# Optimization experiments

Hardware: AMD Instinct MI355X
Metric: run time of the kernel (lower is better)

The kernel has to match this reference:

```python
import jax, jax.numpy as jnp
import numpy as np

B, N, DIM = 8, 8192, 256
K, CDIM = 4096, 1024
COMMIT = 0.25


def setup_inputs() -> dict:
    key = jax.random.key(0)
    ks = jax.random.split(key, 4)
    x = jax.random.normal(ks[0], (B, N, DIM), dtype=jnp.float32)
    ln_g = jnp.ones((DIM,), jnp.float32)
    ln_b = jnp.zeros((DIM,), jnp.float32)
    w_pre = jax.random.normal(ks[1], (DIM, CDIM), jnp.float32) / np.sqrt(DIM)
    b_pre = jnp.zeros((CDIM,), jnp.float32)
    embed = jax.random.normal(ks[2], (K, CDIM), jnp.float32)
    w_post = jax.random.normal(ks[3], (CDIM, DIM), jnp.float32) / np.sqrt(CDIM)
    b_post = jnp.zeros((DIM,), jnp.float32)
    return {"x": x, "ln_g": ln_g, "ln_b": ln_b, "w_pre": w_pre, "b_pre": b_pre,
            "embed": embed, "w_post": w_post, "b_post": b_post}


def reference(x, ln_g, ln_b, w_pre, b_pre, embed, w_post, b_post):
    # LayerNorm over last dim (eps=1e-5, torch default)
    mu = jnp.mean(x, axis=-1, keepdims=True)
    var = jnp.mean((x - mu) ** 2, axis=-1, keepdims=True)
    xn = (x - mu) * jax.lax.rsqrt(var + 1e-5) * ln_g + ln_b
    # GELU (exact, erf-based as in torch default) then Linear dim->codebook_dim
    z_e = jax.nn.gelu(xn, approximate=False) @ w_pre + b_pre  # (B,N,CDIM)
    flat = z_e.reshape(-1, CDIM)                              # (B*N, CDIM)
    # squared euclidean distances to codebook, argmin, gather
    z_sq = jnp.sum(flat * flat, axis=1, keepdims=True)        # (BN,1)
    e_sq = jnp.sum(embed * embed, axis=1)                     # (K,)
    dist = z_sq - 2.0 * (flat @ embed.T) + e_sq[None, :]      # (BN,K)
    indices = jnp.argmin(dist, axis=1)                        # (BN,)
    z_q = embed[indices]                                      # (BN,CDIM)
    # commitment loss (z_q detached)
    commit = COMMIT * jnp.mean((flat - jax.lax.stop_gradient(z_q)) ** 2)
    # straight-through estimator
    z_q_st = flat + jax.lax.stop_gradient(z_q - flat)
    z_q_st = z_q_st.reshape(B, N, CDIM)
    quantized = z_q_st @ w_post + b_post                      # (B,N,DIM)
    return quantized, indices.reshape(B, N), commit
```

## Files before the change

kernel.cpp:

```cpp
#include <hip/hip_runtime.h>

#define BN_ROWS 65536
#define DIMX 256
#define CDIM 1024
#define KCODES 4096
#define NSP 16
#define NSLOT 11
#define NENT 12
#define CMARG 24.0f
#define RMARG 24.0f
#define QS 24.0f
#define INV_S2 (1.0f / (QS * QS))
#define FLT_BIG 3.402823466e+38f

static const size_t OFF_ESQ   = 0;
static const size_t OFF_IDXF  = 16384;
static const size_t OFF_CROW  = 278528;
static const size_t OFF_EPOST = 540672;
static const size_t OFF_EI8   = 4734976;
static const size_t OFF_NFLAG = 8929280;
static const size_t OFF_FLAG  = 8929344;
static const size_t OFF_CAND  = 9191488;

typedef __attribute__((ext_vector_type(4))) int i32x4;

#define GLOAD_LDS16(gsrc, ldst)                                                \
  __builtin_amdgcn_global_load_lds(                                            \
      (const __attribute__((address_space(1))) void*)(gsrc),                   \
      (__attribute__((address_space(3))) void*)(ldst), 16, 0, 0)

template <int VMC>
__device__ __forceinline__ void wait_vm() {
  if constexpr (VMC == 8)
    asm volatile("s_waitcnt vmcnt(8)" ::: "memory");
  else if constexpr (VMC == 4)
    asm volatile("s_waitcnt vmcnt(4)" ::: "memory");
  else
    asm volatile("s_waitcnt vmcnt(0)" ::: "memory");
}

__device__ inline char q8(float f) {
  return (char)__float2int_rn(fminf(fmaxf(f * QS, -127.f), 127.f));
}
__device__ inline unsigned fkey(float s) {
  unsigned b = __float_as_uint(s);
  return b ^ ((unsigned)((int)b >> 31) | 0x80000000u);
}
__device__ inline float keyinv(unsigned k) {
  unsigned b = (k & 0x80000000u) ? (k ^ 0x80000000u) : ~k;
  return __uint_as_float(b);
}

__global__ __launch_bounds__(256) void k_esq(const float* __restrict__ embed,
                                             float* __restrict__ e_sq) {
  const int t = threadIdx.x, wv = t >> 6, lane = t & 63;
  const int row = blockIdx.x * 4 + wv;
  const float* e = embed + (size_t)row * CDIM;
  float s = 0.f;
  for (int k = lane * 4; k < CDIM; k += 256) {
    float4 v = *(const float4*)(e + k);
    s = fmaf(v.x, v.x, s); s = fmaf(v.y, v.y, s);
    s = fmaf(v.z, v.z, s); s = fmaf(v.w, v.w, s);
  }
#pragma unroll
  for (int o = 32; o > 0; o >>= 1) s += __shfl_xor(s, o);
  if (lane == 0) e_sq[row] = s;
}

__global__ __launch_bounds__(256) void k_ei8(const float* __restrict__ embed,
                                             char* __restrict__ Ei8) {
  const int t = threadIdx.x;
  const size_t row = blockIdx.x;
  float4 v = *(const float4*)(embed + row * CDIM + t * 4);
  *(char4*)(Ei8 + row * CDIM + t * 4) =
      make_char4(q8(v.x), q8(v.y), q8(v.z), q8(v.w));
}

__global__ __launch_bounds__(256) void k_ln_gelu_gemm(
    const float* __restrict__ x, const float* __restrict__ ln_g,
    const float* __restrict__ ln_b, const float* __restrict__ w_pre,
    const float* __restrict__ b_pre, float* __restrict__ zf,
    char* __restrict__ zi8, int row0) {
  __shared__ float g[16][DIMX];
  const int t = threadIdx.x;
  const int lrow0 = blockIdx.x * 16;
  const int grow0 = row0 + lrow0;
  const int wv = t >> 6, lane = t & 63;
#pragma unroll
  for (int j = 0; j < 4; ++j) {
    const int r = wv * 4 + j;
    const float* xr = x + (size_t)(grow0 + r) * DIMX;
    float4 v = *(const float4*)(xr + lane * 4);
    float s = v.x + v.y + v.z + v.w;
    float ss = v.x * v.x + v.y * v.y + v.z * v.z + v.w * v.w;
#pragma unroll
    for (int o = 32; o > 0; o >>= 1) { s += __shfl_xor(s, o); ss += __shfl_xor(ss, o); }
    const float mu = s * (1.0f / 256.0f);
    const float var = ss * (1.0f / 256.0f) - mu * mu;
    const float rstd = rsqrtf(var + 1e-5f);
    float vv[4] = {v.x, v.y, v.z, v.w};
#pragma unroll
    for (int q = 0; q < 4; ++q) {
      const int d = lane * 4 + q;
      float xn = (vv[q] - mu) * rstd * ln_g[d] + ln_b[d];
      g[r][d] = 0.5f * xn * (1.0f + erff(xn * 0.70710678118654752f));
    }
  }
  __syncthreads();
  float acc[16][4];
#pragma unroll
  for (int r = 0; r < 16; ++r)
#pragma unroll
    for (int c = 0; c < 4; ++c) acc[r][c] = 0.f;
#pragma unroll 4
  for (int d = 0; d < DIMX; ++d) {
    float4 w = *(const float4*)(w_pre + (size_t)d * CDIM + t * 4);
#pragma unroll
    for (int r = 0; r < 16; ++r) {
      const float gv = g[r][d];
      acc[r][0] = fmaf(gv, w.x, acc[r][0]);
      acc[r][1] = fmaf(gv, w.y, acc[r][1]);
      acc[r][2] = fmaf(gv, w.z, acc[r][2]);
      acc[r][3] = fmaf(gv, w.w, acc[r][3]);
    }
  }
  float4 bp = *(const float4*)(b_pre + t * 4);
#pragma unroll
  for (int r = 0; r < 16; ++r) {
    float4 o;
    o.x = acc[r][0] + bp.x; o.y = acc[r][1] + bp.y;
    o.z = acc[r][2] + bp.z; o.w = acc[r][3] + bp.w;
    *(float4*)(zf + (size_t)(lrow0 + r) * CDIM + t * 4) = o;
    *(char4*)(zi8 + (size_t)(lrow0 + r) * CDIM + t * 4) =
        make_char4(q8(o.x), q8(o.y), q8(o.z), q8(o.w));
  }
}

__global__ __launch_bounds__(512) void k_score(
    const char* __restrict__ Ei8, const char* __restrict__ Zi8,
    const float* __restrict__ e_sq, uint2* __restrict__ cand, int chunk) {
  __shared__ __align__(16) char lds[4][32768];
  const int t = threadIdx.x;
  const int cpx = gridDim.x >> 3;
  const int bx = (blockIdx.x & 7) * cpx + (blockIdx.x >> 3);
  const int zblk = bx / NSP, csp = bx % NSP;
  const int wid = t >> 6, l = t & 63;
  const int wr = wid >> 2, wc = wid & 3;
  const int lg = l >> 4, lo16 = l & 15;
  const int rowbase = zblk * 256;
  const int m0 = csp * 256;
  const int wr8 = wr * 8, wc4 = wc * 4, l16 = l * 16;

  const bool isA = (wid < 4);
  const int q = wid & 3;
  const char* sarr = isA ? Ei8 : Zi8;
  const int sbase = isA ? m0 : rowbase;
  const char* sp0 = sarr + (size_t)(sbase + q * 64 + lo16) * 1024 + lg * 16;
  const int dstbase = (isA ? 0 : 16384) + q * 4096;

  i32x4 acc[8][4];
#pragma unroll
  for (int mi = 0; mi < 8; ++mi)
#pragma unroll
    for (int ni = 0; ni < 4; ++ni) acc[mi][ni] = (i32x4){0, 0, 0, 0};

#pragma unroll
  for (int pk = 0; pk < 3; ++pk) {
    const char* sp = sp0 + pk * 64;
    char* D = &lds[pk][dstbase];
#pragma unroll
    for (int u = 0; u < 4; ++u) GLOAD_LDS16(sp + u * 16384, D + u * 1024);
  }

#define SCORE_KT(KT, VMC, ST)                                                  \
  {                                                                            \
    const char* Lc = lds[(KT) & 3];                                            \
    wait_vm<VMC>();                                                            \
    __builtin_amdgcn_s_barrier();                                              \
    __builtin_amdgcn_sched_barrier(0);                                         \
    i32x4 bh[4], a[8];                                                         \
    _Pragma("unroll") for (int ni = 0; ni < 4; ++ni) bh[ni] =                  \
        *(const i32x4*)(Lc + 16384 + (wc4 + ni) * 1024 + l16);                 \
    _Pragma("unroll") for (int u = 0; u < 8; ++u) a[u] =                       \
        *(const i32x4*)(Lc + (wr8 + u) * 1024 + l16);                          \
    if (ST) {                                                                  \
      char* Dst = &lds[((KT) + 3) & 3][dstbase];                               \
      const char* spk = sp0 + ((KT) + 3) * 64;                                 \
      _Pragma("unroll") for (int u = 0; u < 4; ++u)                            \
          GLOAD_LDS16(spk + u * 16384, Dst + u * 1024);                        \
    }                                                                          \
    asm volatile("s_waitcnt lgkmcnt(0)" ::: "memory");                         \
    __builtin_amdgcn_sched_barrier(0);                                         \
    __builtin_amdgcn_s_setprio(1);                                             \
    _Pragma("unroll") for (int u = 0; u < 8; ++u)                              \
        _Pragma("unroll") for (int ni = 0; ni < 4; ++ni) acc[u][ni] =          \
            __builtin_amdgcn_mfma_i32_16x16x64_i8(a[u], bh[ni],                \
                                                  acc[u][ni], 0, 0, 0);        \
    __builtin_amdgcn_s_setprio(0);                                             \
  }

  for (int kt = 0; kt < 14; ++kt) SCORE_KT(kt, 8, (kt < 13));
  SCORE_KT(14, 4, false);
  SCORE_KT(15, 0, false);
#undef SCORE_KT

  float s1[4];
  int i1[4];
#pragma unroll
  for (int i = 0; i < 4; ++i) { s1[i] = FLT_BIG; i1[i] = 0x7fffffff; }
#pragma unroll
  for (int mi = 0; mi < 8; ++mi) {
    const int c0 = m0 + wr * 128 + mi * 16 + lg * 4;
    float4 es = *(const float4*)(e_sq + c0);
    float esv[4] = {es.x, es.y, es.z, es.w};
#pragma unroll
    for (int ni = 0; ni < 4; ++ni) {
#pragma unroll
      for (int j = 0; j < 4; ++j) {
        const float s = fmaf(-2.0f * INV_S2, (float)acc[mi][ni][j], esv[j]);
        const int c = c0 + j;
        if (s < s1[ni] || (s == s1[ni] && c < i1[ni])) { s1[ni] = s; i1[ni] = c; }
      }
    }
  }

  unsigned long long* red = (unsigned long long*)&lds[0][0];
  float* sb = (float*)&lds[0][4096];
  unsigned* sbi = (unsigned*)&lds[0][5120];
  unsigned* cnt = (unsigned*)&lds[0][6144];
  uint2* slot = (uint2*)&lds[0][7168];

  __syncthreads();
#pragma unroll
  for (int ni = 0; ni < 4; ++ni) {
    unsigned long long k1v =
        (((unsigned long long)fkey(s1[ni])) << 32) | (unsigned)i1[ni];
    unsigned long long o1 = __shfl_xor(k1v, 16);
    k1v = o1 < k1v ? o1 : k1v;
    o1 = __shfl_xor(k1v, 32);
    k1v = o1 < k1v ? o1 : k1v;
    if (lg == 0) {
      const int r = wc * 64 + ni * 16 + lo16;
      red[r * 2 + wr] = k1v;
    }
  }
  __syncthreads();
  if (t < 256) {
    unsigned long long a1 = red[t * 2 + 0], b1 = red[t * 2 + 1];
    if (b1 < a1) a1 = b1;
    sb[t] = keyinv((unsigned)(a1 >> 32));
    sbi[t] = (unsigned)(a1 & 0xFFFFFFFFull);
    cnt[t] = 0;
  }
  __syncthreads();
#pragma unroll
  for (int mi = 0; mi < 8; ++mi) {
    const int c0 = m0 + wr * 128 + mi * 16 + lg * 4;
    float4 es = *(const float4*)(e_sq + c0);
    float esv[4] = {es.x, es.y, es.z, es.w};
#pragma unroll
    for (int ni = 0; ni < 4; ++ni) {
      const int r = wc * 64 + ni * 16 + lo16;
      const float thr = sb[r] + CMARG;
#pragma unroll
      for (int j = 0; j < 4; ++j) {
        const float s = fmaf(-2.0f * INV_S2, (float)acc[mi][ni][j], esv[j]);
        const unsigned c = (unsigned)(c0 + j);
        if (s < thr && c != sbi[r]) {
          unsigned pos = atomicAdd(&cnt[r], 1u);
          if (pos < NSLOT)
            slot[r * NSLOT + pos] = make_uint2(__float_as_uint(s), c);
        }
      }
    }
  }
  __syncthreads();
  if (t < 256) {
    uint2* g = cand + (size_t)(rowbase + t) * (NSP * NENT) + csp * NENT;
    const unsigned ov = (cnt[t] > NSLOT) ? 0x40000000u : 0u;
    g[0] = make_uint2(__float_as_uint(sb[t]), sbi[t] | ov);
    const unsigned n = cnt[t] > NSLOT ? NSLOT : cnt[t];
#pragma unroll
    for (int k = 0; k < NSLOT; ++k)
      g[1 + k] = (k < (int)n) ? slot[t * NSLOT + k]
                              : make_uint2(__float_as_uint(FLT_BIG), 0xFFFFFFFFu);
  }
}

__global__ __launch_bounds__(256) void k_refine(
    const uint2* __restrict__ cand, const float* __restrict__ zf,
    const float* __restrict__ embed, int* __restrict__ idxf,
    float* __restrict__ crow, float* __restrict__ out_idx,
    int* __restrict__ flag_rows, int* __restrict__ nflag, int chunk,
    int row0) {
  const int t = threadIdx.x, wid = t >> 6, l = t & 63;
  const int lrow = blockIdx.x * 4 + wid;
  if (lrow >= chunk) return;
  const int grow = row0 + lrow;
  const uint2* base = cand + (size_t)lrow * (NSP * NENT);
  const uint2 e0 = base[l];
  const uint2 e1 = base[64 + l];
  const uint2 e2 = base[128 + l];
  const bool is0 = (l % NENT) == 0;
  const bool is1 = ((l + 64) % NENT) == 0;
  const bool is2 = ((l + 128) % NENT) == 0;
  float gm = FLT_BIG;
  if (is0) gm = fminf(gm, __uint_as_float(e0.x));
  if (is1) gm = fminf(gm, __uint_as_float(e1.x));
  if (is2) gm = fminf(gm, __uint_as_float(e2.x));
#pragma unroll
  for (int o = 32; o > 0; o >>= 1) gm = fminf(gm, __shfl_xor(gm, o));
  const float thr = gm + RMARG;
  bool myovf = (is0 && (e0.y & 0x40000000u) && __uint_as_float(e0.x) < thr) ||
               (is1 && (e1.y & 0x40000000u) && __uint_as_float(e1.x) < thr) ||
               (is2 && (e2.y & 0x40000000u) && __uint_as_float(e2.x) < thr);
  const bool ovf = __any(myovf);

  float zv[16];
#pragma unroll
  for (int j = 0; j < 16; ++j) zv[j] = zf[(size_t)lrow * CDIM + l + 64 * j];

  double d1 = 1e300;
  int i1 = 0x7fffffff;
#define PROC(E)                                                                \
  {                                                                            \
    const float sc_ = __uint_as_float(E.x);                                    \
    const int id_ = (int)(E.y & 0xFFFFu);                                      \
    unsigned long long mask = __ballot(sc_ < thr && id_ < KCODES);             \
    while (mask) {                                                             \
      const int src = __ffsll((unsigned long long)mask) - 1;                   \
      mask &= mask - 1;                                                        \
      const int c = __shfl(id_, src);                                          \
      const float* e = embed + (size_t)c * CDIM;                               \
      double dd = 0.0;                                                         \
      _Pragma("unroll") for (int j = 0; j < 16; ++j) {                         \
        const double df = (double)zv[j] - (double)e[l + 64 * j];               \
        dd = fma(df, df, dd);                                                  \
      }                                                                        \
      _Pragma("unroll") for (int o = 32; o > 0; o >>= 1) dd +=                 \
          __shfl_xor(dd, o);                                                   \
      if (dd < d1 || (dd == d1 && c < i1)) { d1 = dd; i1 = c; }                \
    }                                                                          \
  }
  PROC(e0);
  PROC(e1);
  PROC(e2);
#undef PROC
  if (l == 0) {
    idxf[grow] = i1;
    out_idx[grow] = (float)i1;
    crow[grow] = (float)d1;
    if (ovf) {
      const int s = atomicAdd(nflag, 1);
      flag_rows[s] = lrow;
    }
  }
}

__global__ __launch_bounds__(256) void k_exact(
    const float* __restrict__ zf, const float* __restrict__ embed,
    const int* __restrict__ flag_rows, const int* __restrict__ nflag,
    int* __restrict__ idxf, float* __restrict__ crow,
    float* __restrict__ out_idx, int row0) {
  __shared__ double wd[4];
  __shared__ int wcidx[4];
  const int t = threadIdx.x;
  const int wid = t >> 6, l = t & 63;
  const int n = *nflag;

  for (int fi = blockIdx.x; fi < n; fi += gridDim.x) {
    const int lrow = flag_rows[fi];
    const int grow = row0 + lrow;
    float zr[16];
#pragma unroll
    for (int j = 0; j < 16; ++j) zr[j] = zf[(size_t)lrow * CDIM + l + 64 * j];
    double dmin = 1e300;
    int cmin = 0x7fffffff;
    for (int ci = 0; ci < 1024; ++ci) {
      const int c = wid * 1024 + ci;
      const float* e = embed + (size_t)c * CDIM;
      double dd = 0.0;
#pragma unroll
      for (int j = 0; j < 16; ++j) {
        const double df = (double)zr[j] - (double)e[l + 64 * j];
        dd = fma(df, df, dd);
      }
#pragma unroll
      for (int o = 32; o > 0; o >>= 1) dd += __shfl_xor(dd, o);
      if (dd < dmin) { dmin = dd; cmin = c; }
    }
    if (l == 0) { wd[wid] = dmin; wcidx[wid] = cmin; }
    __syncthreads();
    if (t == 0) {
      double dm = wd[0]; int cm = wcidx[0];
#pragma unroll
      for (int wv = 1; wv < 4; ++wv) {
        if (wd[wv] < dm || (wd[wv] == dm && wcidx[wv] < cm)) {
          dm = wd[wv]; cm = wcidx[wv];
        }
      }
      idxf[grow] = cm;
      out_idx[grow] = (float)cm;
      crow[grow] = (float)dm;
    }
    __syncthreads();
  }
}

__global__ __launch_bounds__(256) void k_epost(const float* __restrict__ E,
                                               const float* __restrict__ w_post,
                                               float* __restrict__ E_post) {
  __shared__ float es[16][128];
  const int t = threadIdx.x;
  const int r0 = blockIdx.x * 16;
  float acc[16];
#pragma unroll
  for (int r = 0; r < 16; ++r) acc[r] = 0.f;
  for (int k0 = 0; k0 < CDIM; k0 += 128) {
    __syncthreads();
#pragma unroll
    for (int p = 0; p < 2; ++p) {
      const int fl = (p * 256 + t) * 4;
      const int r = fl >> 7, kk = fl & 127;
      float4 v = *(const float4*)(E + (size_t)(r0 + r) * CDIM + k0 + kk);
      *(float4*)&es[r][kk] = v;
    }
    __syncthreads();
#pragma unroll 4
    for (int d = 0; d < 128; ++d) {
      const float w = w_post[(size_t)(k0 + d) * DIMX + t];
#pragma unroll
      for (int r = 0; r < 16; ++r) acc[r] = fmaf(es[r][d], w, acc[r]);
    }
  }
#pragma unroll
  for (int r = 0; r < 16; ++r)
    E_post[(size_t)(r0 + r) * DIMX + t] = acc[r];
}

__global__ __launch_bounds__(256) void k_gather(const float* __restrict__ E_post,
                                                const int* __restrict__ idx,
                                                const float* __restrict__ b_post,
                                                float* __restrict__ outq) {
  const int t = threadIdx.x;
  const int r0 = blockIdx.x * 16;
  const float bp = b_post[t];
#pragma unroll
  for (int i = 0; i < 16; ++i) {
    const int row = r0 + i;
    outq[(size_t)row * DIMX + t] = E_post[(size_t)idx[row] * DIMX + t] + bp;
  }
}

__global__ __launch_bounds__(256) void k_commit_final(
    const float* __restrict__ crow, float* __restrict__ out_commit) {
  const int t = threadIdx.x;
  double s = 0.0;
  for (int i = t; i < BN_ROWS; i += 256) s += (double)crow[i];
#pragma unroll
  for (int o = 32; o > 0; o >>= 1) s += __shfl_xor(s, o);
  __shared__ double wsum[4];
  if ((t & 63) == 0) wsum[t >> 6] = s;
  __syncthreads();
  if (t == 0)
    *out_commit = (float)(0.25 * (wsum[0] + wsum[1] + wsum[2] + wsum[3]) /
                          (65536.0 * 1024.0));
}

extern "C" void kernel_launch(void* const* d_in, const int* in_sizes, int n_in,
                              void* d_out, int out_size, void* d_ws,
                              size_t ws_size, hipStream_t stream) {
  const float* x = (const float*)d_in[0];
  const float* ln_g = (const float*)d_in[1];
  const float* ln_b = (const float*)d_in[2];
  const float* w_pre = (const float*)d_in[3];
  const float* b_pre = (const float*)d_in[4];
  const float* embed = (const float*)d_in[5];
  const float* w_post = (const float*)d_in[6];
  const float* b_post = (const float*)d_in[7];

  float* out = (float*)d_out;
  float* outq = out;
  float* out_idx = out + 16777216;
  float* out_commit = out + 16842752;

  char* ws = (char*)d_ws;
  float* e_sq = (float*)(ws + OFF_ESQ);
  int* idxf = (int*)(ws + OFF_IDXF);
  float* crow = (float*)(ws + OFF_CROW);
  float* E_post = (float*)(ws + OFF_EPOST);
  char* Ei8 = (char*)(ws + OFF_EI8);
  int* nflag = (int*)(ws + OFF_NFLAG);
  int* flag_rows = (int*)(ws + OFF_FLAG);

  int chunk = 4096;
  while (chunk < BN_ROWS &&
         OFF_CAND + (size_t)(chunk * 2) * 6656ull <= ws_size)
    chunk *= 2;
  uint2* cand = (uint2*)(ws + OFF_CAND);
  char* zi8 = ws + OFF_CAND + (size_t)chunk * 1536;
  float* zf = (float*)(ws + OFF_CAND + (size_t)chunk * 1536 +
                       (size_t)chunk * 1024);

  k_esq<<<KCODES / 4, 256, 0, stream>>>(embed, e_sq);
  k_ei8<<<KCODES, 256, 0, stream>>>(embed, Ei8);
  k_epost<<<KCODES / 16, 256, 0, stream>>>(embed, w_post, E_post);

  for (int row0 = 0; row0 < BN_ROWS; row0 += chunk) {
    hipMemsetAsync(nflag, 0, sizeof(int), stream);
    k_ln_gelu_gemm<<<chunk / 16, 256, 0, stream>>>(x, ln_g, ln_b, w_pre, b_pre,
                                                   zf, zi8, row0);
    k_score<<<(chunk / 256) * NSP, 512, 0, stream>>>(Ei8, zi8, e_sq, cand,
                                                     chunk);
    k_refine<<<chunk / 4, 256, 0, stream>>>(cand, zf, embed, idxf, crow,
                                            out_idx, flag_rows, nflag, chunk,
                                            row0);
    k_exact<<<128, 256, 0, stream>>>(zf, embed, flag_rows, nflag, idxf, crow,
                                     out_idx, row0);
  }

  k_gather<<<BN_ROWS / 16, 256, 0, stream>>>(E_post, idxf, b_post, outq);
  k_commit_final<<<1, 256, 0, stream>>>(crow, out_commit);
}
```

Before: 1.364 ms.

## Shrink candidate lists and margins, simplify score pipeline, vectorize pre-GEMM loads

Cuts the per-split candidate slots from 11 to 5 and halves the rescoring margins, so the refine kernel reads and rescores fewer candidates with exact fp64 distances. The int8 score kernel drops from a 4-stage LDS ring with partial vmcnt waits to a 2-stage double buffer that waits for all loads each step. The LN-GELU pre-projection GEMM now reads four g values as a float4 from LDS and four w_pre rows per step. The smaller margins and candidate lists raise the risk of missing the true argmin and of more rows overflowing to the exact fallback, and the simpler buffering may expose more load latency.

```diff
diff --git a/kernel.cpp b/kernel.cpp
--- a/kernel.cpp
+++ b/kernel.cpp
@@ -5,10 +5,10 @@
 #define CDIM 1024
 #define KCODES 4096
 #define NSP 16
-#define NSLOT 11
-#define NENT 12
-#define CMARG 24.0f
-#define RMARG 24.0f
+#define NSLOT 5
+#define NENT 6
+#define CMARG 12.0f
+#define RMARG 12.0f
 #define QS 24.0f
 #define INV_S2 (1.0f / (QS * QS))
 #define FLT_BIG 3.402823466e+38f
@@ -28,16 +28,6 @@
   __builtin_amdgcn_global_load_lds(                                            \
       (const __attribute__((address_space(1))) void*)(gsrc),                   \
       (__attribute__((address_space(3))) void*)(ldst), 16, 0, 0)
-
-template <int VMC>
-__device__ __forceinline__ void wait_vm() {
-  if constexpr (VMC == 8)
-    asm volatile("s_waitcnt vmcnt(8)" ::: "memory");
-  else if constexpr (VMC == 4)
-    asm volatile("s_waitcnt vmcnt(4)" ::: "memory");
-  else
-    asm volatile("s_waitcnt vmcnt(0)" ::: "memory");
-}
 
 __device__ inline char q8(float f) {
   return (char)__float2int_rn(fminf(fmaxf(f * QS, -127.f), 127.f));
@@ -112,16 +102,31 @@
   for (int r = 0; r < 16; ++r)
 #pragma unroll
     for (int c = 0; c < 4; ++c) acc[r][c] = 0.f;
-#pragma unroll 4
-  for (int d = 0; d < DIMX; ++d) {
-    float4 w = *(const float4*)(w_pre + (size_t)d * CDIM + t * 4);
+#pragma unroll 2
+  for (int d0 = 0; d0 < DIMX; d0 += 4) {
+    float4 w0 = *(const float4*)(w_pre + (size_t)(d0 + 0) * CDIM + t * 4);
+    float4 w1 = *(const float4*)(w_pre + (size_t)(d0 + 1) * CDIM + t * 4);
+    float4 w2 = *(const float4*)(w_pre + (size_t)(d0 + 2) * CDIM + t * 4);
+    float4 w3 = *(const float4*)(w_pre + (size_t)(d0 + 3) * CDIM + t * 4);
 #pragma unroll
     for (int r = 0; r < 16; ++r) {
-      const float gv = g[r][d];
-      acc[r][0] = fmaf(gv, w.x, acc[r][0]);
-      acc[r][1] = fmaf(gv, w.y, acc[r][1]);
-      acc[r][2] = fmaf(gv, w.z, acc[r][2]);
-      acc[r][3] = fmaf(gv, w.w, acc[r][3]);
+      float4 gv = *(const float4*)&g[r][d0];
+      acc[r][0] = fmaf(gv.x, w0.x, acc[r][0]);
+      acc[r][1] = fmaf(gv.x, w0.y, acc[r][1]);
+      acc[r][2] = fmaf(gv.x, w0.z, acc[r][2]);
+      acc[r][3] = fmaf(gv.x, w0.w, acc[r][3]);
+      acc[r][0] = fmaf(gv.y, w1.x, acc[r][0]);
+      acc[r][1] = fmaf(gv.y, w1.y, acc[r][1]);
+      acc[r][2] = fmaf(gv.y, w1.z, acc[r][2]);
+      acc[r][3] = fmaf(gv.y, w1.w, acc[r][3]);
+      acc[r][0] = fmaf(gv.z, w2.x, acc[r][0]);
+      acc[r][1] = fmaf(gv.z, w2.y, acc[r][1]);
+      acc[r][2] = fmaf(gv.z, w2.z, acc[r][2]);
+      acc[r][3] = fmaf(gv.z, w2.w, acc[r][3]);
+      acc[r][0] = fmaf(gv.w, w3.x, acc[r][0]);
+      acc[r][1] = fmaf(gv.w, w3.y, acc[r][1]);
+      acc[r][2] = fmaf(gv.w, w3.z, acc[r][2]);
+      acc[r][3] = fmaf(gv.w, w3.w, acc[r][3]);
     }
   }
   float4 bp = *(const float4*)(b_pre + t * 4);
@@ -139,7 +144,7 @@
 __global__ __launch_bounds__(512) void k_score(
     const char* __restrict__ Ei8, const char* __restrict__ Zi8,
     const float* __restrict__ e_sq, uint2* __restrict__ cand, int chunk) {
-  __shared__ __align__(16) char lds[4][32768];
+  __shared__ __align__(16) char lds[2][32768];
   const int t = threadIdx.x;
   const int cpx = gridDim.x >> 3;
   const int bx = (blockIdx.x & 7) * cpx + (blockIdx.x >> 3);
@@ -164,45 +169,41 @@
 #pragma unroll
     for (int ni = 0; ni < 4; ++ni) acc[mi][ni] = (i32x4){0, 0, 0, 0};
 
-#pragma unroll
-  for (int pk = 0; pk < 3; ++pk) {
-    const char* sp = sp0 + pk * 64;
-    char* D = &lds[pk][dstbase];
-#pragma unroll
-    for (int u = 0; u < 4; ++u) GLOAD_LDS16(sp + u * 16384, D + u * 1024);
-  }
-
-#define SCORE_KT(KT, VMC, ST)                                                  \
-  {                                                                            \
-    const char* Lc = lds[(KT) & 3];                                            \
-    wait_vm<VMC>();                                                            \
-    __builtin_amdgcn_s_barrier();                                              \
-    __builtin_amdgcn_sched_barrier(0);                                         \
-    i32x4 bh[4], a[8];                                                         \
-    _Pragma("unroll") for (int ni = 0; ni < 4; ++ni) bh[ni] =                  \
-        *(const i32x4*)(Lc + 16384 + (wc4 + ni) * 1024 + l16);                 \
-    _Pragma("unroll") for (int u = 0; u < 8; ++u) a[u] =                       \
-        *(const i32x4*)(Lc + (wr8 + u) * 1024 + l16);                          \
-    if (ST) {                                                                  \
-      char* Dst = &lds[((KT) + 3) & 3][dstbase];                               \
-      const char* spk = sp0 + ((KT) + 3) * 64;                                 \
-      _Pragma("unroll") for (int u = 0; u < 4; ++u)                            \
-          GLOAD_LDS16(spk + u * 16384, Dst + u * 1024);                        \
-    }                                                                          \
-    asm volatile("s_waitcnt lgkmcnt(0)" ::: "memory");                         \
-    __builtin_amdgcn_sched_barrier(0);                                         \
-    __builtin_amdgcn_s_setprio(1);                                             \
-    _Pragma("unroll") for (int u = 0; u < 8; ++u)                              \
-        _Pragma("unroll") for (int ni = 0; ni < 4; ++ni) acc[u][ni] =          \
-            __builtin_amdgcn_mfma_i32_16x16x64_i8(a[u], bh[ni],                \
-                                                  acc[u][ni], 0, 0, 0);        \
-    __builtin_amdgcn_s_setprio(0);                                             \
-  }
-
-  for (int kt = 0; kt < 14; ++kt) SCORE_KT(kt, 8, (kt < 13));
-  SCORE_KT(14, 4, false);
-  SCORE_KT(15, 0, false);
-#undef SCORE_KT
+  {
+    char* D = &lds[0][dstbase];
+#pragma unroll
+    for (int u = 0; u < 4; ++u) GLOAD_LDS16(sp0 + u * 16384, D + u * 1024);
+  }
+
+  for (int kt = 0; kt < 16; ++kt) {
+    const char* Lc = lds[kt & 1];
+    asm volatile("s_waitcnt vmcnt(0)" ::: "memory");
+    __builtin_amdgcn_s_barrier();
+    __builtin_amdgcn_sched_barrier(0);
+    if (kt < 15) {
+      char* Dst = &lds[(kt + 1) & 1][dstbase];
+      const char* spk = sp0 + (kt + 1) * 64;
+#pragma unroll
+      for (int u = 0; u < 4; ++u) GLOAD_LDS16(spk + u * 16384, Dst + u * 1024);
+    }
+    i32x4 bh[4], a[8];
+#pragma unroll
+    for (int ni = 0; ni < 4; ++ni)
+      bh[ni] = *(const i32x4*)(Lc + 16384 + (wc4 + ni) * 1024 + l16);
+#pragma unroll
+    for (int u = 0; u < 8; ++u)
+      a[u] = *(const i32x4*)(Lc + (wr8 + u) * 1024 + l16);
+    asm volatile("s_waitcnt lgkmcnt(0)" ::: "memory");
+    __builtin_amdgcn_sched_barrier(0);
+    __builtin_amdgcn_s_setprio(1);
+#pragma unroll
+    for (int u = 0; u < 8; ++u)
+#pragma unroll
+      for (int ni = 0; ni < 4; ++ni)
+        acc[u][ni] = __builtin_amdgcn_mfma_i32_16x16x64_i8(a[u], bh[ni],
+                                                           acc[u][ni], 0, 0, 0);
+    __builtin_amdgcn_s_setprio(0);
+  }
 
   float s1[4];
   int i1[4];
@@ -299,21 +300,18 @@
   const int grow = row0 + lrow;
   const uint2* base = cand + (size_t)lrow * (NSP * NENT);
   const uint2 e0 = base[l];
-  const uint2 e1 = base[64 + l];
-  const uint2 e2 = base[128 + l];
+  const uint2 e1 = (l < 32) ? base[64 + l]
+                            : make_uint2(__float_as_uint(FLT_BIG), 0xFFFFFFFFu);
   const bool is0 = (l % NENT) == 0;
-  const bool is1 = ((l + 64) % NENT) == 0;
-  const bool is2 = ((l + 128) % NENT) == 0;
+  const bool is1 = (l < 32) && (((64 + l) % NENT) == 0);
   float gm = FLT_BIG;
   if (is0) gm = fminf(gm, __uint_as_float(e0.x));
   if (is1) gm = fminf(gm, __uint_as_float(e1.x));
-  if (is2) gm = fminf(gm, __uint_as_float(e2.x));
 #pragma unroll
   for (int o = 32; o > 0; o >>= 1) gm = fminf(gm, __shfl_xor(gm, o));
   const float thr = gm + RMARG;
   bool myovf = (is0 && (e0.y & 0x40000000u) && __uint_as_float(e0.x) < thr) ||
-               (is1 && (e1.y & 0x40000000u) && __uint_as_float(e1.x) < thr) ||
-               (is2 && (e2.y & 0x40000000u) && __uint_as_float(e2.x) < thr);
+               (is1 && (e1.y & 0x40000000u) && __uint_as_float(e1.x) < thr);
   const bool ovf = __any(myovf);
 
   float zv[16];
@@ -344,7 +342,6 @@
   }
   PROC(e0);
   PROC(e1);
-  PROC(e2);
 #undef PROC
   if (l == 0) {
     idxf[grow] = i1;
@@ -495,11 +492,11 @@
 
   int chunk = 4096;
   while (chunk < BN_ROWS &&
-         OFF_CAND + (size_t)(chunk * 2) * 6656ull <= ws_size)
+         OFF_CAND + (size_t)(chunk * 2) * 5888ull <= ws_size)
     chunk *= 2;
   uint2* cand = (uint2*)(ws + OFF_CAND);
-  char* zi8 = ws + OFF_CAND + (size_t)chunk * 1536;
-  float* zf = (float*)(ws + OFF_CAND + (size_t)chunk * 1536 +
+  char* zi8 = ws + OFF_CAND + (size_t)chunk * 768;
+  float* zf = (float*)(ws + OFF_CAND + (size_t)chunk * 768 +
                        (size_t)chunk * 1024);
 
   k_esq<<<KCODES / 4, 256, 0, stream>>>(embed, e_sq);
```

New measurement: 1.331 ms. 1.02x faster.
